# Kernel tuning notes

Hardware: AMD Instinct MI355X
Metric: run time of the kernel (lower is better)

Reference implementation:

```python
import jax, jax.numpy as jnp
import numpy as np

C, K, D = 64, 512, 2048   # classes, shots per class, hidden_dim
N_ITER = 3                # n_routing_iter


def _squash(x):
    # x: (..., d); squash along last axis: x * ||x|| / (1 + ||x||^2)
    n2 = jnp.sum(x * x, axis=-1, keepdims=True)
    n = jnp.sqrt(n2)
    return x * (n / (1.0 + n2))


def setup_inputs() -> dict:
    key = jax.random.key(0)
    z_s = jax.random.normal(key, (C, K, D), dtype=jnp.float32)
    return {"z_s": z_s}


def reference(z_s):
    # z_s: (C, K, D). All C classes routed in parallel (vectorized over the
    # original Python loop over classes).
    z_sq = _squash(z_s)                       # (C, K, D)
    b = jnp.zeros(z_s.shape[:2], z_s.dtype)   # routing logits (C, K)
    c = jnp.zeros((z_s.shape[0], z_s.shape[2]), z_s.dtype)
    for _ in range(N_ITER):
        d = jax.nn.softmax(b, axis=-1)                      # (C, K)
        c = _squash(jnp.einsum('ck,ckd->cd', d, z_sq))      # (C, D)
        b = b + jnp.einsum('ckd,cd->ck', z_sq, c)           # (C, K)
    # returned representative is c from the LAST iteration (b update after is unused,
    # matching the torch loop where c_i from the final iter is appended)
    return c
```

## Files before the change

kernel.cpp:

```cpp
#include <hip/hip_runtime.h>
#include <hip/hip_fp16.h>
#include <math.h>

#define C_CLS   64
#define K_SHOTS 512
#define D_DIM   2048
#define BPC     16
#define ROWS_PER_BLOCK (K_SHOTS / BPC)
#define NWAVES  4
#define ROWS_PER_WAVE (ROWS_PER_BLOCK / NWAVES)
#define NBLK    (C_CLS * BPC)
#define NF4     8
#define NH4     4

typedef float v4f __attribute__((ext_vector_type(4)));

__device__ __forceinline__ float4 ntload4(const float* p) {
    v4f v = __builtin_nontemporal_load((const v4f*)p);
    float4 r; r.x = v.x; r.y = v.y; r.z = v.z; r.w = v.w; return r;
}

__device__ __forceinline__ uint2 pack4(float4 v) {
    union { uint2 u; __half2 h[2]; } pk;
    pk.h[0] = __floats2half2_rn(v.x, v.y);
    pk.h[1] = __floats2half2_rn(v.z, v.w);
    return pk.u;
}

__device__ __forceinline__ float wave_reduce_sum(float v) {
#pragma unroll
    for (int off = 32; off > 0; off >>= 1)
        v += __shfl_xor(v, off, 64);
    return v;
}

__global__ __launch_bounds__(256)
void route_pass0(const float* __restrict__ z,
                 __half* __restrict__ z16,
                 float* __restrict__ part_s,
                 float* __restrict__ part_e)
{
    __shared__ float4 s_comb[NWAVES][D_DIM / 4];
    __shared__ float  e_comb[NWAVES];

    const int blk  = blockIdx.x;
    const int cls  = blk >> 4;
    const int bic  = blk & (BPC - 1);
    const int lane = threadIdx.x & 63;
    const int wid  = threadIdx.x >> 6;
    const int t    = threadIdx.x;

    float4 acc[NF4];
#pragma unroll
    for (int i = 0; i < NF4; ++i) acc[i] = make_float4(0.f, 0.f, 0.f, 0.f);
    float esum = 0.f;

    const int k0 = bic * ROWS_PER_BLOCK + wid * ROWS_PER_WAVE;
    const float* __restrict__ zb = z + ((size_t)cls * K_SHOTS + k0) * D_DIM;

    float4 zcur[NF4];
#pragma unroll
    for (int i = 0; i < NF4; ++i) zcur[i] = ntload4(zb + 4 * (lane + i * 64));

#pragma unroll
    for (int r = 0; r < ROWS_PER_WAVE; ++r) {
        float4 znext[NF4];
        if (r + 1 < ROWS_PER_WAVE) {
            const float* zn = zb + (size_t)(r + 1) * D_DIM;
#pragma unroll
            for (int i = 0; i < NF4; ++i) znext[i] = ntload4(zn + 4 * (lane + i * 64));
        }
        float n2 = 0.f;
#pragma unroll
        for (int i = 0; i < NF4; ++i)
            n2 += zcur[i].x * zcur[i].x + zcur[i].y * zcur[i].y
                + zcur[i].z * zcur[i].z + zcur[i].w * zcur[i].w;
        n2 = wave_reduce_sum(n2);
        const float sc = sqrtf(n2) / (1.f + n2);

        uint2* p16 = (uint2*)(z16 + ((size_t)cls * K_SHOTS + k0 + r) * D_DIM);
#pragma unroll
        for (int i = 0; i < NF4; ++i) {
            float4 s;
            s.x = sc * zcur[i].x; s.y = sc * zcur[i].y;
            s.z = sc * zcur[i].z; s.w = sc * zcur[i].w;
            p16[lane + i * 64] = pack4(s);
            acc[i].x += s.x; acc[i].y += s.y; acc[i].z += s.z; acc[i].w += s.w;
        }
        esum += 1.f;

        if (r + 1 < ROWS_PER_WAVE) {
#pragma unroll
            for (int i = 0; i < NF4; ++i) zcur[i] = znext[i];
        }
    }

#pragma unroll
    for (int i = 0; i < NF4; ++i) s_comb[wid][lane + i * 64] = acc[i];
    if (lane == 0) e_comb[wid] = esum;
    __syncthreads();

    float4* ps = (float4*)(part_s + (size_t)blk * D_DIM);
#pragma unroll
    for (int j = 0; j < 2; ++j) {
        const int f = t + j * 256;
        const float4 a  = s_comb[0][f];
        const float4 b4 = s_comb[1][f];
        const float4 c4 = s_comb[2][f];
        const float4 d4 = s_comb[3][f];
        float4 s;
        s.x = (a.x + b4.x) + (c4.x + d4.x);
        s.y = (a.y + b4.y) + (c4.y + d4.y);
        s.z = (a.z + b4.z) + (c4.z + d4.z);
        s.w = (a.w + b4.w) + (c4.w + d4.w);
        ps[f] = s;
    }
    if (t == 0) part_e[blk] = (e_comb[0] + e_comb[1]) + (e_comb[2] + e_comb[3]);
}

template <int PASS>
__global__ __launch_bounds__(256)
void route_pass_h(const __half* __restrict__ z16,
                  float* __restrict__ bvec,
                  const float* __restrict__ c_prev,
                  float* __restrict__ part_s,
                  float* __restrict__ part_e)
{
    __shared__ float4 s_comb[NWAVES][D_DIM / 4];
    __shared__ float  e_comb[NWAVES];

    const int rawblk = blockIdx.x;
    const int blk  = (PASS == 1) ? (NBLK - 1 - rawblk) : rawblk;
    const int cls  = blk >> 4;
    const int bic  = blk & (BPC - 1);
    const int lane = threadIdx.x & 63;
    const int wid  = threadIdx.x >> 6;
    const int t    = threadIdx.x;

    const float4* cp4 = (const float4*)(c_prev + (size_t)cls * D_DIM);
    float4 cpA[NH4], cpB[NH4];
#pragma unroll
    for (int j = 0; j < NH4; ++j) {
        const int c2i = 2 * (lane + j * 64);
        cpA[j] = cp4[c2i];
        cpB[j] = cp4[c2i + 1];
    }

    float4 acc[2 * NH4];
#pragma unroll
    for (int i = 0; i < 2 * NH4; ++i) acc[i] = make_float4(0.f, 0.f, 0.f, 0.f);
    float esum = 0.f;

    const int k0 = bic * ROWS_PER_BLOCK + wid * ROWS_PER_WAVE;
    const float4* __restrict__ zb =
        (const float4*)(z16 + ((size_t)cls * K_SHOTS + k0) * D_DIM);

    const int r0    = (PASS == 1) ? (ROWS_PER_WAVE - 1) : 0;
    const int rstep = (PASS == 1) ? -1 : 1;

    float4 zcur[NH4];
#pragma unroll
    for (int j = 0; j < NH4; ++j)
        zcur[j] = zb[(size_t)r0 * (D_DIM / 8) + lane + j * 64];

#pragma unroll
    for (int rr = 0; rr < ROWS_PER_WAVE; ++rr) {
        const int r = r0 + rr * rstep;
        float4 znext[NH4];
        if (rr + 1 < ROWS_PER_WAVE) {
            const float4* zn = zb + (size_t)(r + rstep) * (D_DIM / 8);
#pragma unroll
            for (int j = 0; j < NH4; ++j) znext[j] = zn[lane + j * 64];
        }

        float dot = 0.f;
#pragma unroll
        for (int j = 0; j < NH4; ++j) {
            const __half2* hp = (const __half2*)&zcur[j];
            const float2 a0 = __half22float2(hp[0]);
            const float2 a1 = __half22float2(hp[1]);
            const float2 a2 = __half22float2(hp[2]);
            const float2 a3 = __half22float2(hp[3]);
            dot += a0.x * cpA[j].x + a0.y * cpA[j].y
                 + a1.x * cpA[j].z + a1.y * cpA[j].w
                 + a2.x * cpB[j].x + a2.y * cpB[j].y
                 + a3.x * cpB[j].z + a3.y * cpB[j].w;
        }
        dot = wave_reduce_sum(dot);

        const int k = k0 + r;
        float bnew = dot;
        if (PASS == 2) bnew += bvec[cls * K_SHOTS + k];
        if (PASS == 1 && lane == 0) bvec[cls * K_SHOTS + k] = bnew;
        const float w = expf(bnew);
        esum += w;

#pragma unroll
        for (int j = 0; j < NH4; ++j) {
            const __half2* hp = (const __half2*)&zcur[j];
            const float2 a0 = __half22float2(hp[0]);
            const float2 a1 = __half22float2(hp[1]);
            const float2 a2 = __half22float2(hp[2]);
            const float2 a3 = __half22float2(hp[3]);
            acc[2 * j].x     += w * a0.x;  acc[2 * j].y     += w * a0.y;
            acc[2 * j].z     += w * a1.x;  acc[2 * j].w     += w * a1.y;
            acc[2 * j + 1].x += w * a2.x;  acc[2 * j + 1].y += w * a2.y;
            acc[2 * j + 1].z += w * a3.x;  acc[2 * j + 1].w += w * a3.y;
        }

        if (rr + 1 < ROWS_PER_WAVE) {
#pragma unroll
            for (int j = 0; j < NH4; ++j) zcur[j] = znext[j];
        }
    }

#pragma unroll
    for (int j = 0; j < NH4; ++j) {
        const int c2i = 2 * (lane + j * 64);
        s_comb[wid][c2i]     = acc[2 * j];
        s_comb[wid][c2i + 1] = acc[2 * j + 1];
    }
    if (lane == 0) e_comb[wid] = esum;
    __syncthreads();

    float4* ps = (float4*)(part_s + (size_t)blk * D_DIM);
#pragma unroll
    for (int j = 0; j < 2; ++j) {
        const int f = t + j * 256;
        const float4 a  = s_comb[0][f];
        const float4 b4 = s_comb[1][f];
        const float4 c4 = s_comb[2][f];
        const float4 d4 = s_comb[3][f];
        float4 s;
        s.x = (a.x + b4.x) + (c4.x + d4.x);
        s.y = (a.y + b4.y) + (c4.y + d4.y);
        s.z = (a.z + b4.z) + (c4.z + d4.z);
        s.w = (a.w + b4.w) + (c4.w + d4.w);
        ps[f] = s;
    }
    if (t == 0) part_e[blk] = (e_comb[0] + e_comb[1]) + (e_comb[2] + e_comb[3]);
}

__global__ __launch_bounds__(256)
void reduce_squash(const float* __restrict__ part_s,
                   const float* __restrict__ part_e,
                   float* __restrict__ c_out)
{
    __shared__ float wred[NWAVES];
    const int cls  = blockIdx.x;
    const int t    = threadIdx.x;
    const int lane = t & 63;
    const int wid  = t >> 6;

    float esum = 0.f;
#pragma unroll
    for (int p = 0; p < BPC; ++p) esum += part_e[cls * BPC + p];
    const float inv = 1.f / esum;

    float4 m[2];
    float n2p = 0.f;
#pragma unroll
    for (int j = 0; j < 2; ++j) {
        const int f = t + j * 256;
        float4 s = make_float4(0.f, 0.f, 0.f, 0.f);
        for (int p = 0; p < BPC; ++p) {
            const float4 v =
                ((const float4*)(part_s + (size_t)(cls * BPC + p) * D_DIM))[f];
            s.x += v.x; s.y += v.y; s.z += v.z; s.w += v.w;
        }
        m[j].x = s.x * inv; m[j].y = s.y * inv;
        m[j].z = s.z * inv; m[j].w = s.w * inv;
        n2p += m[j].x * m[j].x + m[j].y * m[j].y
             + m[j].z * m[j].z + m[j].w * m[j].w;
    }
    float n2 = wave_reduce_sum(n2p);
    if (lane == 0) wred[wid] = n2;
    __syncthreads();
    n2 = (wred[0] + wred[1]) + (wred[2] + wred[3]);
    const float fac = sqrtf(n2) / (1.f + n2);

    float4* co = (float4*)(c_out + (size_t)cls * D_DIM);
#pragma unroll
    for (int j = 0; j < 2; ++j) {
        const int f = t + j * 256;
        float4 o;
        o.x = m[j].x * fac; o.y = m[j].y * fac;
        o.z = m[j].z * fac; o.w = m[j].w * fac;
        co[f] = o;
    }
}

extern "C" void kernel_launch(void* const* d_in, const int* in_sizes, int n_in,
                              void* d_out, int out_size, void* d_ws, size_t ws_size,
                              hipStream_t stream)
{
    const float* z = (const float*)d_in[0];
    float* out = (float*)d_out;
    float* ws  = (float*)d_ws;

    float* bvec   = ws;
    float* c_buf  = bvec + C_CLS * K_SHOTS;
    float* part_s = c_buf + (size_t)C_CLS * D_DIM;
    float* part_e = part_s + (size_t)NBLK * D_DIM;
    __half* z16   = (__half*)(part_e + NBLK);

    route_pass0<<<NBLK, 256, 0, stream>>>(z, z16, part_s, part_e);
    reduce_squash<<<C_CLS, 256, 0, stream>>>(part_s, part_e, c_buf);

    route_pass_h<1><<<NBLK, 256, 0, stream>>>(z16, bvec, c_buf, part_s, part_e);
    reduce_squash<<<C_CLS, 256, 0, stream>>>(part_s, part_e, c_buf);

    route_pass_h<2><<<NBLK, 256, 0, stream>>>(z16, bvec, c_buf, part_s, part_e);
    reduce_squash<<<C_CLS, 256, 0, stream>>>(part_s, part_e, out);
}
```

Baseline: 151.6 us.

## Fuse reduce-squash into routing passes and drop constant softmax denominator

Removes two reduce_squash launches by having every routing-pass block redundantly reduce the 16 per-class partial sums and squash them into c in shared memory before its main loop. Pass 0 no longer tracks the exp-sum because with zero logits it always equals K, so pass 1 uses the constant directly. Partial buffers are double-buffered so a pass reads one set and writes the other. The cost is that each of the 16 blocks per class rereads 16×D partial floats, adding redundant L2 traffic and extra barriers in exchange for fewer launch gaps.

```diff
diff --git a/kernel.cpp b/kernel.cpp
--- a/kernel.cpp
+++ b/kernel.cpp
@@ -37,11 +37,9 @@
 __global__ __launch_bounds__(256)
 void route_pass0(const float* __restrict__ z,
                  __half* __restrict__ z16,
-                 float* __restrict__ part_s,
-                 float* __restrict__ part_e)
+                 float* __restrict__ part_s)
 {
     __shared__ float4 s_comb[NWAVES][D_DIM / 4];
-    __shared__ float  e_comb[NWAVES];
 
     const int blk  = blockIdx.x;
     const int cls  = blk >> 4;
@@ -53,7 +51,6 @@
     float4 acc[NF4];
 #pragma unroll
     for (int i = 0; i < NF4; ++i) acc[i] = make_float4(0.f, 0.f, 0.f, 0.f);
-    float esum = 0.f;
 
     const int k0 = bic * ROWS_PER_BLOCK + wid * ROWS_PER_WAVE;
     const float* __restrict__ zb = z + ((size_t)cls * K_SHOTS + k0) * D_DIM;
@@ -87,8 +84,6 @@
             p16[lane + i * 64] = pack4(s);
             acc[i].x += s.x; acc[i].y += s.y; acc[i].z += s.z; acc[i].w += s.w;
         }
-        esum += 1.f;
-
         if (r + 1 < ROWS_PER_WAVE) {
 #pragma unroll
             for (int i = 0; i < NF4; ++i) zcur[i] = znext[i];
@@ -97,7 +92,6 @@
 
 #pragma unroll
     for (int i = 0; i < NF4; ++i) s_comb[wid][lane + i * 64] = acc[i];
-    if (lane == 0) e_comb[wid] = esum;
     __syncthreads();
 
     float4* ps = (float4*)(part_s + (size_t)blk * D_DIM);
@@ -115,16 +109,16 @@
         s.w = (a.w + b4.w) + (c4.w + d4.w);
         ps[f] = s;
     }
-    if (t == 0) part_e[blk] = (e_comb[0] + e_comb[1]) + (e_comb[2] + e_comb[3]);
 }
 
 template <int PASS>
 __global__ __launch_bounds__(256)
 void route_pass_h(const __half* __restrict__ z16,
                   float* __restrict__ bvec,
-                  const float* __restrict__ c_prev,
-                  float* __restrict__ part_s,
-                  float* __restrict__ part_e)
+                  const float* __restrict__ ps_in,
+                  const float* __restrict__ pe_in,
+                  float* __restrict__ ps_out,
+                  float* __restrict__ pe_out)
 {
     __shared__ float4 s_comb[NWAVES][D_DIM / 4];
     __shared__ float  e_comb[NWAVES];
@@ -137,20 +131,6 @@
     const int wid  = threadIdx.x >> 6;
     const int t    = threadIdx.x;
 
-    const float4* cp4 = (const float4*)(c_prev + (size_t)cls * D_DIM);
-    float4 cpA[NH4], cpB[NH4];
-#pragma unroll
-    for (int j = 0; j < NH4; ++j) {
-        const int c2i = 2 * (lane + j * 64);
-        cpA[j] = cp4[c2i];
-        cpB[j] = cp4[c2i + 1];
-    }
-
-    float4 acc[2 * NH4];
-#pragma unroll
-    for (int i = 0; i < 2 * NH4; ++i) acc[i] = make_float4(0.f, 0.f, 0.f, 0.f);
-    float esum = 0.f;
-
     const int k0 = bic * ROWS_PER_BLOCK + wid * ROWS_PER_WAVE;
     const float4* __restrict__ zb =
         (const float4*)(z16 + ((size_t)cls * K_SHOTS + k0) * D_DIM);
@@ -162,6 +142,62 @@
 #pragma unroll
     for (int j = 0; j < NH4; ++j)
         zcur[j] = zb[(size_t)r0 * (D_DIM / 8) + lane + j * 64];
+
+    float esum_prev;
+    if (PASS == 1) {
+        esum_prev = (float)K_SHOTS;
+    } else {
+        esum_prev = 0.f;
+#pragma unroll
+        for (int p = 0; p < BPC; ++p) esum_prev += pe_in[cls * BPC + p];
+    }
+    const float inv = 1.f / esum_prev;
+
+    float4 m[2];
+    float n2p = 0.f;
+#pragma unroll
+    for (int j = 0; j < 2; ++j) {
+        const int f = t + j * 256;
+        float4 s = make_float4(0.f, 0.f, 0.f, 0.f);
+#pragma unroll
+        for (int p = 0; p < BPC; ++p) {
+            const float4 v =
+                ((const float4*)(ps_in + (size_t)(cls * BPC + p) * D_DIM))[f];
+            s.x += v.x; s.y += v.y; s.z += v.z; s.w += v.w;
+        }
+        m[j].x = s.x * inv; m[j].y = s.y * inv;
+        m[j].z = s.z * inv; m[j].w = s.w * inv;
+        n2p += m[j].x * m[j].x + m[j].y * m[j].y
+             + m[j].z * m[j].z + m[j].w * m[j].w;
+    }
+    float n2 = wave_reduce_sum(n2p);
+    if (lane == 0) e_comb[wid] = n2;
+    __syncthreads();
+    n2 = (e_comb[0] + e_comb[1]) + (e_comb[2] + e_comb[3]);
+    const float fac = sqrtf(n2) / (1.f + n2);
+#pragma unroll
+    for (int j = 0; j < 2; ++j) {
+        const int f = t + j * 256;
+        float4 cv;
+        cv.x = m[j].x * fac; cv.y = m[j].y * fac;
+        cv.z = m[j].z * fac; cv.w = m[j].w * fac;
+        s_comb[0][f] = cv;
+    }
+    __syncthreads();
+
+    float4 cpA[NH4], cpB[NH4];
+#pragma unroll
+    for (int j = 0; j < NH4; ++j) {
+        const int c2i = 2 * (lane + j * 64);
+        cpA[j] = s_comb[0][c2i];
+        cpB[j] = s_comb[0][c2i + 1];
+    }
+    __syncthreads();
+
+    float4 acc[2 * NH4];
+#pragma unroll
+    for (int i = 0; i < 2 * NH4; ++i) acc[i] = make_float4(0.f, 0.f, 0.f, 0.f);
+    float esum = 0.f;
 
 #pragma unroll
     for (int rr = 0; rr < ROWS_PER_WAVE; ++rr) {
@@ -223,7 +259,7 @@
     if (lane == 0) e_comb[wid] = esum;
     __syncthreads();
 
-    float4* ps = (float4*)(part_s + (size_t)blk * D_DIM);
+    float4* ps = (float4*)(ps_out + (size_t)blk * D_DIM);
 #pragma unroll
     for (int j = 0; j < 2; ++j) {
         const int f = t + j * 256;
@@ -238,7 +274,7 @@
         s.w = (a.w + b4.w) + (c4.w + d4.w);
         ps[f] = s;
     }
-    if (t == 0) part_e[blk] = (e_comb[0] + e_comb[1]) + (e_comb[2] + e_comb[3]);
+    if (t == 0) pe_out[blk] = (e_comb[0] + e_comb[1]) + (e_comb[2] + e_comb[3]);
 }
 
 __global__ __launch_bounds__(256)
@@ -298,18 +334,17 @@
     float* out = (float*)d_out;
     float* ws  = (float*)d_ws;
 
-    float* bvec   = ws;
-    float* c_buf  = bvec + C_CLS * K_SHOTS;
-    float* part_s = c_buf + (size_t)C_CLS * D_DIM;
-    float* part_e = part_s + (size_t)NBLK * D_DIM;
-    __half* z16   = (__half*)(part_e + NBLK);
-
-    route_pass0<<<NBLK, 256, 0, stream>>>(z, z16, part_s, part_e);
-    reduce_squash<<<C_CLS, 256, 0, stream>>>(part_s, part_e, c_buf);
-
-    route_pass_h<1><<<NBLK, 256, 0, stream>>>(z16, bvec, c_buf, part_s, part_e);
-    reduce_squash<<<C_CLS, 256, 0, stream>>>(part_s, part_e, c_buf);
-
-    route_pass_h<2><<<NBLK, 256, 0, stream>>>(z16, bvec, c_buf, part_s, part_e);
-    reduce_squash<<<C_CLS, 256, 0, stream>>>(part_s, part_e, out);
-}
+    float* bvec    = ws;
+    float* part_s0 = bvec + C_CLS * K_SHOTS;
+    float* part_s1 = part_s0 + (size_t)NBLK * D_DIM;
+    float* part_e1 = part_s1 + (size_t)NBLK * D_DIM;
+    float* part_e2 = part_e1 + NBLK;
+    __half* z16    = (__half*)(part_e2 + NBLK);
+
+    route_pass0<<<NBLK, 256, 0, stream>>>(z, z16, part_s0);
+    route_pass_h<1><<<NBLK, 256, 0, stream>>>(z16, bvec, part_s0, nullptr,
+                                              part_s1, part_e1);
+    route_pass_h<2><<<NBLK, 256, 0, stream>>>(z16, bvec, part_s1, part_e1,
+                                              part_s0, part_e2);
+    reduce_squash<<<C_CLS, 256, 0, stream>>>(part_s0, part_e2, out);
+}
```

Measured after the change: 181.4 us. 19.6% more time.
